# Kernel tuning notes

Hardware: AMD Instinct MI355X
Metric: run time of the kernel (lower is better)

## Reference

```python
import jax, jax.numpy as jnp
import numpy as np

VOCAB = 50000
E = 300        # embedding_dim
HID = 512      # hidden_dim (bidirectional total)
HD = HID // 2  # per-direction hidden
K = 20         # tagset size
START = 18
STOP = 19
B = 64
T = 256
NEG = -10000.0


def setup_inputs() -> dict:
    key = jax.random.key(0)
    ks = jax.random.split(key, 12)
    s = 0.1
    sentence = jax.random.randint(ks[0], (B, T), 0, VOCAB)
    length = jax.random.randint(ks[1], (B,), T // 2, T + 1)
    embed_table = jax.random.normal(ks[2], (VOCAB, E)) * s
    w_ih_f = jax.random.normal(ks[3], (4 * HD, E)) * s
    w_hh_f = jax.random.normal(ks[4], (4 * HD, HD)) * s
    b_f = jax.random.normal(ks[5], (4 * HD,)) * s
    w_ih_b = jax.random.normal(ks[6], (4 * HD, E)) * s
    w_hh_b = jax.random.normal(ks[7], (4 * HD, HD)) * s
    b_b = jax.random.normal(ks[8], (4 * HD,)) * s
    W_out = jax.random.normal(ks[9], (K, HID)) * s
    b_out = jax.random.normal(ks[10], (K,)) * s
    transitions = jax.random.normal(ks[11], (K, K))
    transitions = transitions.at[START, :].set(NEG).at[:, STOP].set(NEG)
    return dict(sentence=sentence, length=length, embed_table=embed_table,
                w_ih_f=w_ih_f, w_hh_f=w_hh_f, b_f=b_f,
                w_ih_b=w_ih_b, w_hh_b=w_hh_b, b_b=b_b,
                W_out=W_out, b_out=b_out, transitions=transitions)


def _lstm(xs, w_ih, w_hh, b, reverse):
    # xs: [T, B, E]; PyTorch gate order i, f, g, o
    Bn = xs.shape[1]
    H = w_hh.shape[1]

    def step(carry, x):
        h, c = carry
        g = x @ w_ih.T + h @ w_hh.T + b
        i, f, gg, o = jnp.split(g, 4, axis=-1)
        c = jax.nn.sigmoid(f) * c + jax.nn.sigmoid(i) * jnp.tanh(gg)
        h = jax.nn.sigmoid(o) * jnp.tanh(c)
        return (h, c), h

    init = (jnp.zeros((Bn, H), xs.dtype), jnp.zeros((Bn, H), xs.dtype))
    _, hs = jax.lax.scan(step, init, xs, reverse=reverse)
    return hs  # [T, B, H], time-ordered


def _viterbi(feats, length, transitions):
    # feats: [B, T, K]; vectorized over batch, scan over time
    Bn, Tn, Kn = feats.shape
    fv0 = jnp.full((Bn, Kn), NEG, feats.dtype).at[:, START].set(0.0)
    idk = jnp.arange(Kn)

    def step(fv, inp):
        feat_t, t = inp
        # scores[b, next, prev] = fv[b, prev] + transitions[next, prev]
        sc = fv[:, None, :] + transitions[None, :, :]
        bp = jnp.argmax(sc, axis=-1)              # [B, K]
        best = jnp.max(sc, axis=-1) + feat_t      # [B, K]
        m = (t < length)[:, None]
        fv_new = jnp.where(m, best, fv)           # freeze past sentence end
        bp = jnp.where(m, bp, idk[None, :])       # identity backpointer on pad
        return fv_new, bp

    fv, bps = jax.lax.scan(step, fv0, (jnp.swapaxes(feats, 0, 1), jnp.arange(Tn)))
    term = fv + transitions[STOP][None, :]
    last = jnp.argmax(term, axis=-1)              # [B]
    score = jnp.max(term, axis=-1)                # [B] viterbi max score

    def back(tag, bp_t):
        prev = jnp.take_along_axis(bp_t, tag[:, None], axis=1)[:, 0]
        return prev, tag

    _, path_t = jax.lax.scan(back, last, bps, reverse=True)  # [T, B], time order
    path = jnp.swapaxes(path_t, 0, 1)             # [B, T]; entries >= length repeat last tag
    return score, path


def reference(sentence, length, embed_table, w_ih_f, w_hh_f, b_f,
              w_ih_b, w_hh_b, b_b, W_out, b_out, transitions):
    embeds = embed_table[sentence]                # [B, T, E]
    xs = jnp.swapaxes(embeds, 0, 1)               # [T, B, E]
    hf = _lstm(xs, w_ih_f, w_hh_f, b_f, reverse=False)
    hb = _lstm(xs, w_ih_b, w_hh_b, b_b, reverse=True)
    h = jnp.concatenate([hf, hb], axis=-1)        # [T, B, HID]
    feats = h @ W_out.T + b_out                   # [T, B, K]
    feats = jnp.swapaxes(feats, 0, 1)             # [B, T, K]
    score, path = _viterbi(feats, length, transitions)
    return score, path
```

## Files before the change

kernel.cpp:

```cpp
#include <hip/hip_runtime.h>
#include <hip/hip_bf16.h>

#define DINL __device__ __forceinline__

namespace {

typedef unsigned long long u64;

constexpr int Tn = 256;
constexpr int Bn = 64;
constexpr int HDn = 256;
constexpr int Kt = 20;
constexpr int STOPt = 19;
constexpr int STARTt = 18;
constexpr float NEGV = -10000.0f;

DINL float sigm(float x) { return 1.0f / (1.0f + __expf(-x)); }
DINL float tanh_f(float x) {
  float ax = fabsf(x);
  float e = __expf(-2.0f * ax);
  float t = (1.0f - e) / (1.0f + e);
  return x < 0.0f ? -t : t;
}

__global__ void k_clear(int4* p) {
  int i = threadIdx.x;
  p[i] = {0, 0, 0, 0};
}

__global__ void k_wt(const float* __restrict__ wf, const float* __restrict__ wb,
                     float* __restrict__ Wt) {
  int idx = blockIdx.x * 256 + threadIdx.x;
  if (idx >= 300 * 2048) return;
  int k = idx >> 11, n = idx & 2047;
  const float* w = (n < 1024) ? wf : wb;
  int nn = n & 1023;
  Wt[idx] = w[nn * 300 + k];
}

__global__ __launch_bounds__(256) void k_xproj(
    const int* __restrict__ sentence, const float* __restrict__ table,
    const float* __restrict__ Wt, const float* __restrict__ b_f,
    const float* __restrict__ b_b, float* __restrict__ xproj) {
  __shared__ float As[20][68];
  __shared__ float Bs[20][136];
  __shared__ int tok[64];

  int tid = threadIdx.x;
  int t = blockIdx.x;
  int n0 = blockIdx.y * 128;

  if (tid < 64) tok[tid] = sentence[tid * Tn + t];
  __syncthreads();

  int ty = tid >> 4, tx = tid & 15;
  float acc[4][8];
#pragma unroll
  for (int i = 0; i < 4; ++i)
#pragma unroll
    for (int j = 0; j < 8; ++j) acc[i][j] = 0.0f;

  for (int k0 = 0; k0 < 300; k0 += 20) {
#pragma unroll
    for (int i = 0; i < 5; ++i) {
      int idx = i * 256 + tid;
      int r = idx / 20, kk = idx % 20;
      As[kk][r] = table[tok[r] * 300 + k0 + kk];
    }
#pragma unroll
    for (int i = 0; i < 10; ++i) {
      int idx = i * 256 + tid;
      int kk = idx >> 7, c = idx & 127;
      Bs[kk][c] = Wt[(k0 + kk) * 2048 + n0 + c];
    }
    __syncthreads();
#pragma unroll
    for (int kk = 0; kk < 20; ++kk) {
      float4 a4 = *(const float4*)&As[kk][ty * 4];
      float4 b4a = *(const float4*)&Bs[kk][tx * 8];
      float4 b4b = *(const float4*)&Bs[kk][tx * 8 + 4];
      float av[4] = {a4.x, a4.y, a4.z, a4.w};
      float bvv[8] = {b4a.x, b4a.y, b4a.z, b4a.w, b4b.x, b4b.y, b4b.z, b4b.w};
#pragma unroll
      for (int i = 0; i < 4; ++i)
#pragma unroll
        for (int j = 0; j < 8; ++j) acc[i][j] += av[i] * bvv[j];
    }
    __syncthreads();
  }

  float bias[8];
#pragma unroll
  for (int j = 0; j < 8; ++j) {
    int n = n0 + tx * 8 + j;
    bias[j] = (n < 1024) ? b_f[n] : b_b[n - 1024];
  }
#pragma unroll
  for (int i = 0; i < 4; ++i) {
    size_t m = (size_t)t * 64 + ty * 4 + i;
    float* dst = &xproj[m * 2048 + n0 + tx * 8];
    float4 v0 = {acc[i][0] + bias[0], acc[i][1] + bias[1], acc[i][2] + bias[2],
                 acc[i][3] + bias[3]};
    float4 v1 = {acc[i][4] + bias[4], acc[i][5] + bias[5], acc[i][6] + bias[6],
                 acc[i][7] + bias[7]};
    *(float4*)dst = v0;
    *(float4*)(dst + 4) = v1;
  }
}

__global__ __launch_bounds__(128) void k_lstm(
    const float* __restrict__ whh_f, const float* __restrict__ whh_b,
    const float* __restrict__ xproj, float* __restrict__ h_all,
    int* __restrict__ flags) {
  __shared__ __align__(16) float hl[16 * 256];

  int tid = threadIdx.x;
  int bid = blockIdx.x;
  int gid = bid & 7;
  int s = bid >> 3;
  int dir = gid >> 2;
  int bg = gid & 3;
  const float* whh = dir ? whh_b : whh_f;

  int c = tid >> 4;
  int kc = tid & 15;

  float4 w4[4][4];
#pragma unroll
  for (int g = 0; g < 4; ++g) {
    const float* src = whh + ((size_t)(g * 256 + s * 8 + c)) * 256;
#pragma unroll
    for (int jj = 0; jj < 4; ++jj)
      w4[g][jj] = *(const float4*)(src + ((kc + (jj << 4)) << 2));
  }

  float c_reg = 0.0f;

  for (int st = 0; st < Tn; ++st) {
    int xt = dir ? (Tn - 1 - st) : st;

    float xp[4];
    {
      size_t base = ((size_t)(xt * 64 + bg * 16 + kc)) * 2048 + dir * 1024 +
                    s * 8 + c;
#pragma unroll
      for (int g = 0; g < 4; ++g) xp[g] = xproj[base + g * 256];
    }

    float acc[16][4];
#pragma unroll
    for (int b = 0; b < 16; ++b)
#pragma unroll
      for (int g = 0; g < 4; ++g) acc[b][g] = 0.0f;

    if (st > 0) {
      if (tid < 64) {
        const int* fp = flags + ((gid << 5) + (tid & 31)) * 4;
        for (;;) {
          int v = __hip_atomic_load(fp, __ATOMIC_RELAXED,
                                    __HIP_MEMORY_SCOPE_AGENT);
          if (__all((tid < 32) ? (v >= st) : 1)) break;
          __builtin_amdgcn_s_sleep(1);
        }
      }
      __syncthreads();

      int pt = dir ? (xt + 1) : (xt - 1);
      const float* hsrc =
          h_all + ((size_t)(dir * Tn + pt) * 64 + bg * 16) * 256;
      const char* tb = (const char*)hsrc + (size_t)tid * 16;
      const char* p0 = tb;
      const char* p1 = tb + 4096;
      const char* p2 = tb + 8192;
      const char* p3 = tb + 12288;
      float4 q0, q1, q2, q3, q4, q5, q6, q7;
      asm volatile(
          "global_load_dwordx4 %0, %8, off sc1\n\t"
          "global_load_dwordx4 %1, %8, off offset:2048 sc1\n\t"
          "global_load_dwordx4 %2, %9, off sc1\n\t"
          "global_load_dwordx4 %3, %9, off offset:2048 sc1\n\t"
          "global_load_dwordx4 %4, %10, off sc1\n\t"
          "global_load_dwordx4 %5, %10, off offset:2048 sc1\n\t"
          "global_load_dwordx4 %6, %11, off sc1\n\t"
          "global_load_dwordx4 %7, %11, off offset:2048 sc1\n\t"
          "s_waitcnt vmcnt(0)"
          : "=&v"(q0), "=&v"(q1), "=&v"(q2), "=&v"(q3), "=&v"(q4), "=&v"(q5),
            "=&v"(q6), "=&v"(q7)
          : "v"(p0), "v"(p1), "v"(p2), "v"(p3));
      *(float4*)&hl[(tid + 0 * 128) << 2] = q0;
      *(float4*)&hl[(tid + 1 * 128) << 2] = q1;
      *(float4*)&hl[(tid + 2 * 128) << 2] = q2;
      *(float4*)&hl[(tid + 3 * 128) << 2] = q3;
      *(float4*)&hl[(tid + 4 * 128) << 2] = q4;
      *(float4*)&hl[(tid + 5 * 128) << 2] = q5;
      *(float4*)&hl[(tid + 6 * 128) << 2] = q6;
      *(float4*)&hl[(tid + 7 * 128) << 2] = q7;
      __syncthreads();

#pragma unroll
      for (int b = 0; b < 16; ++b) {
#pragma unroll
        for (int jj = 0; jj < 4; ++jj) {
          float4 hv = *(const float4*)&hl[b * 256 + ((kc + (jj << 4)) << 2)];
#pragma unroll
          for (int g = 0; g < 4; ++g) {
            acc[b][g] += w4[g][jj].x * hv.x + w4[g][jj].y * hv.y +
                         w4[g][jj].z * hv.z + w4[g][jj].w * hv.w;
          }
        }
      }
    }

#pragma unroll
    for (int r = 0; r < 4; ++r) {
      int m = 1 << r;
      int kb = (kc >> r) & 1;
#pragma unroll
      for (int ii = 0; ii < (16 >> (r + 1)); ++ii) {
#pragma unroll
        for (int g = 0; g < 4; ++g) {
          float e = acc[2 * ii][g], o = acc[2 * ii + 1][g];
          float kept = kb ? o : e;
          float sent = kb ? e : o;
          acc[ii][g] = kept + __shfl_xor(sent, m, 64);
        }
      }
    }

    {
      float gi = acc[0][0] + xp[0];
      float gf = acc[0][1] + xp[1];
      float gg = acc[0][2] + xp[2];
      float go = acc[0][3] + xp[3];
      c_reg = sigm(gf) * c_reg + sigm(gi) * tanh_f(gg);
      float h = sigm(go) * tanh_f(c_reg);
      __hip_atomic_store(
          &h_all[((size_t)(dir * Tn + xt) * 64 + bg * 16 + kc) * 256 + s * 8 +
                 c],
          h, __ATOMIC_RELAXED, __HIP_MEMORY_SCOPE_AGENT);
    }

    asm volatile("s_waitcnt vmcnt(0)" ::: "memory");
    __syncthreads();
    if (tid == 0) {
      __hip_atomic_store(flags + ((gid << 5) + s) * 4, st + 1,
                         __ATOMIC_RELAXED, __HIP_MEMORY_SCOPE_AGENT);
    }
  }
}

__global__ __launch_bounds__(256) void k_feats(const float* __restrict__ h_all,
                                               const float* __restrict__ Wout,
                                               const float* __restrict__ bout,
                                               float* __restrict__ feats) {
  __shared__ float Wl[20 * 512];
  __shared__ float hlf[64 * 256];

  int tid = threadIdx.x;
  int t = blockIdx.x;
  for (int i = tid; i < 20 * 512; i += 256) Wl[i] = Wout[i];

  float acc[5] = {0, 0, 0, 0, 0};
  int b = tid & 63, kg5 = tid >> 6;
  int swz = b & 7;

  for (int d = 0; d < 2; ++d) {
    __syncthreads();
    const float* hsrc = h_all + ((size_t)(d * Tn + t)) * 64 * 256;
#pragma unroll 8
    for (int i = 0; i < 64; ++i) {
      int idx = i * 256 + tid;
      int hb = idx >> 8, k = idx & 255;
      hlf[hb * 256 + 4 * ((k >> 2) ^ (hb & 7)) + (k & 3)] = hsrc[idx];
    }
    __syncthreads();
    for (int jg = 0; jg < 64; ++jg) {
      float4 hv = *(const float4*)&hlf[b * 256 + 4 * (jg ^ swz)];
#pragma unroll
      for (int kk = 0; kk < 5; ++kk) {
        int krow = kg5 * 5 + kk;
        float4 wvv = *(const float4*)&Wl[krow * 512 + d * 256 + jg * 4];
        acc[kk] += hv.x * wvv.x + hv.y * wvv.y + hv.z * wvv.z + hv.w * wvv.w;
      }
    }
  }
#pragma unroll
  for (int kk = 0; kk < 5; ++kk) {
    int krow = kg5 * 5 + kk;
    feats[((size_t)b * Tn + t) * Kt + krow] = acc[kk] + bout[krow];
  }
}

__global__ __launch_bounds__(64) void k_viterbi(const float* __restrict__ feats,
                                                const float* __restrict__ trans,
                                                const int* __restrict__ length,
                                                float* __restrict__ out) {
  __shared__ float tr[400];
  __shared__ float fv[20];
  __shared__ float term[20];
  __shared__ unsigned char bps[256][20];

  int b = blockIdx.x;
  int lane = threadIdx.x;
  for (int i = lane; i < 400; i += 64) tr[i] = trans[i];
  if (lane < 20) fv[lane] = (lane == STARTt) ? 0.0f : NEGV;
  int len = length[b];
  __syncthreads();

  for (int t = 0; t < Tn; ++t) {
    float nf = 0.0f;
    int bp = 0;
    if (lane < 20) {
      if (t < len) {
        float vmax = -3.4e38f;
        int pb = 0;
#pragma unroll
        for (int p = 0; p < 20; ++p) {
          float v = fv[p] + tr[lane * 20 + p];
          if (v > vmax) { vmax = v; pb = p; }
        }
        nf = vmax + feats[((size_t)b * Tn + t) * Kt + lane];
        bp = pb;
      } else {
        nf = fv[lane];
        bp = lane;
      }
    }
    __syncthreads();
    if (lane < 20) {
      fv[lane] = nf;
      bps[t][lane] = (unsigned char)bp;
    }
    __syncthreads();
  }

  if (lane < 20) term[lane] = fv[lane] + tr[STOPt * 20 + lane];
  __syncthreads();
  if (lane == 0) {
    float smax = term[0];
    int last = 0;
    for (int p = 1; p < 20; ++p)
      if (term[p] > smax) { smax = term[p]; last = p; }
    out[b] = smax;
    int tag = last;
    for (int t = Tn - 1; t >= 0; --t) {
      out[64 + b * Tn + t] = (float)tag;
      tag = bps[t][tag];
    }
  }
}

}

extern "C" void kernel_launch(void* const* d_in, const int* in_sizes, int n_in,
                              void* d_out, int out_size, void* d_ws,
                              size_t ws_size, hipStream_t stream) {
  const int* sentence = (const int*)d_in[0];
  const int* length = (const int*)d_in[1];
  const float* table = (const float*)d_in[2];
  const float* w_ih_f = (const float*)d_in[3];
  const float* w_hh_f = (const float*)d_in[4];
  const float* b_f = (const float*)d_in[5];
  const float* w_ih_b = (const float*)d_in[6];
  const float* w_hh_b = (const float*)d_in[7];
  const float* b_b = (const float*)d_in[8];
  const float* W_out = (const float*)d_in[9];
  const float* b_out = (const float*)d_in[10];
  const float* trans = (const float*)d_in[11];
  float* out = (float*)d_out;

  float* ws = (float*)d_ws;
  float* xproj = ws;
  float* h_all = ws + (size_t)33554432;
  float* Wt = h_all + (size_t)8388608;
  float* feats = Wt + (size_t)300 * 2048;
  int* flags = (int*)(feats + (size_t)Bn * Tn * Kt);
  (void)ws_size; (void)in_sizes; (void)n_in; (void)out_size;

  k_clear<<<dim3(1), dim3(512), 0, stream>>>((int4*)flags);
  k_wt<<<dim3(2400), dim3(256), 0, stream>>>(w_ih_f, w_ih_b, Wt);
  k_xproj<<<dim3(256, 16), dim3(256), 0, stream>>>(sentence, table, Wt, b_f,
                                                   b_b, xproj);
  k_lstm<<<dim3(256), dim3(128), 0, stream>>>(w_hh_f, w_hh_b, xproj, h_all,
                                              flags);
  k_feats<<<dim3(256), dim3(256), 0, stream>>>(h_all, W_out, b_out, feats);
  k_viterbi<<<dim3(64), dim3(64), 0, stream>>>(feats, trans, length, out);
}
```

Before: 1.750 ms.

## Use epoch-based flags and plain stores when a sync group shares one XCD

Each LSTM block reads its hardware XCD id and publishes it in a table tagged with a per-launch epoch counter. The 32 blocks of a sync group check whether they all landed on the same XCD, and if so they write h values and progress flags with plain stores instead of agent-scope atomic stores. The flag-clearing kernel is replaced by an epoch increment with epoch-offset flag values, which removes the memset launch. This adds a startup handshake per block and depends on plain stores being visible within one XCD's L2, which is a correctness risk.

```diff
diff --git a/kernel.cpp b/kernel.cpp
--- a/kernel.cpp
+++ b/kernel.cpp
@@ -23,9 +23,9 @@
   return x < 0.0f ? -t : t;
 }
 
-__global__ void k_clear(int4* p) {
-  int i = threadIdx.x;
-  p[i] = {0, 0, 0, 0};
+__global__ void k_epoch(unsigned* ep) {
+  if (threadIdx.x == 0)
+    __hip_atomic_fetch_add(ep, 1u, __ATOMIC_RELAXED, __HIP_MEMORY_SCOPE_AGENT);
 }
 
 __global__ void k_wt(const float* __restrict__ wf, const float* __restrict__ wb,
@@ -111,8 +111,10 @@
 __global__ __launch_bounds__(128) void k_lstm(
     const float* __restrict__ whh_f, const float* __restrict__ whh_b,
     const float* __restrict__ xproj, float* __restrict__ h_all,
-    int* __restrict__ flags) {
+    int* __restrict__ flags, int* __restrict__ xcdtab,
+    const unsigned* __restrict__ ep) {
   __shared__ __align__(16) float hl[16 * 256];
+  __shared__ int fastsh;
 
   int tid = threadIdx.x;
   int bid = blockIdx.x;
@@ -125,6 +127,31 @@
   int c = tid >> 4;
   int kc = tid & 15;
 
+  unsigned E =
+      __hip_atomic_load(ep, __ATOMIC_RELAXED, __HIP_MEMORY_SCOPE_AGENT);
+  unsigned xcd = __builtin_amdgcn_s_getreg((3 << 11) | (0 << 6) | 20) & 0xFu;
+  if (tid == 0) {
+    __hip_atomic_store(&xcdtab[(gid << 5) + s],
+                       (int)((E << 4) | xcd), __ATOMIC_RELAXED,
+                       __HIP_MEMORY_SCOPE_AGENT);
+  }
+  if (tid < 64) {
+    const int* xp_ = xcdtab + (gid << 5) + (tid & 31);
+    unsigned v;
+    for (;;) {
+      v = (unsigned)__hip_atomic_load(xp_, __ATOMIC_RELAXED,
+                                      __HIP_MEMORY_SCOPE_AGENT);
+      bool rdy = (v >> 4) == (E & 0x0FFFFFFFu);
+      if (__all((tid < 32) ? rdy : 1)) break;
+      __builtin_amdgcn_s_sleep(1);
+    }
+    int mine = (int)(v & 0xFu);
+    int ref = __shfl(mine, 0, 64);
+    bool eq = (mine == ref);
+    bool alleq = __all((tid < 32) ? eq : 1);
+    if (tid == 0) fastsh = alleq ? 1 : 0;
+  }
+
   float4 w4[4][4];
 #pragma unroll
   for (int g = 0; g < 4; ++g) {
@@ -134,6 +161,10 @@
       w4[g][jj] = *(const float4*)(src + ((kc + (jj << 4)) << 2));
   }
 
+  __syncthreads();
+  const bool fast = (fastsh != 0);
+  const unsigned base = E * 256u;
+
   float c_reg = 0.0f;
 
   for (int st = 0; st < Tn; ++st) {
@@ -141,10 +172,10 @@
 
     float xp[4];
     {
-      size_t base = ((size_t)(xt * 64 + bg * 16 + kc)) * 2048 + dir * 1024 +
-                    s * 8 + c;
-#pragma unroll
-      for (int g = 0; g < 4; ++g) xp[g] = xproj[base + g * 256];
+      size_t xb = ((size_t)(xt * 64 + bg * 16 + kc)) * 2048 + dir * 1024 +
+                  s * 8 + c;
+#pragma unroll
+      for (int g = 0; g < 4; ++g) xp[g] = xproj[xb + g * 256];
     }
 
     float acc[16][4];
@@ -157,9 +188,10 @@
       if (tid < 64) {
         const int* fp = flags + ((gid << 5) + (tid & 31)) * 4;
         for (;;) {
-          int v = __hip_atomic_load(fp, __ATOMIC_RELAXED,
-                                    __HIP_MEMORY_SCOPE_AGENT);
-          if (__all((tid < 32) ? (v >= st) : 1)) break;
+          unsigned v = (unsigned)__hip_atomic_load(
+              fp, __ATOMIC_RELAXED, __HIP_MEMORY_SCOPE_AGENT);
+          int d = (int)(v - base);
+          if (__all((tid < 32) ? (d >= st) : 1)) break;
           __builtin_amdgcn_s_sleep(1);
         }
       }
@@ -234,17 +266,26 @@
       float go = acc[0][3] + xp[3];
       c_reg = sigm(gf) * c_reg + sigm(gi) * tanh_f(gg);
       float h = sigm(go) * tanh_f(c_reg);
-      __hip_atomic_store(
-          &h_all[((size_t)(dir * Tn + xt) * 64 + bg * 16 + kc) * 256 + s * 8 +
-                 c],
-          h, __ATOMIC_RELAXED, __HIP_MEMORY_SCOPE_AGENT);
+      size_t hi = ((size_t)(dir * Tn + xt) * 64 + bg * 16 + kc) * 256 + s * 8 +
+                  c;
+      if (fast) {
+        h_all[hi] = h;
+      } else {
+        __hip_atomic_store(&h_all[hi], h, __ATOMIC_RELAXED,
+                           __HIP_MEMORY_SCOPE_AGENT);
+      }
     }
 
     asm volatile("s_waitcnt vmcnt(0)" ::: "memory");
     __syncthreads();
     if (tid == 0) {
-      __hip_atomic_store(flags + ((gid << 5) + s) * 4, st + 1,
-                         __ATOMIC_RELAXED, __HIP_MEMORY_SCOPE_AGENT);
+      int fv = (int)(base + (unsigned)(st + 1));
+      if (fast) {
+        flags[((gid << 5) + s) * 4] = fv;
+      } else {
+        __hip_atomic_store(flags + ((gid << 5) + s) * 4, fv, __ATOMIC_RELAXED,
+                           __HIP_MEMORY_SCOPE_AGENT);
+      }
     }
   }
 }
@@ -375,14 +416,16 @@
   float* Wt = h_all + (size_t)8388608;
   float* feats = Wt + (size_t)300 * 2048;
   int* flags = (int*)(feats + (size_t)Bn * Tn * Kt);
+  int* xcdtab = flags + 1024;
+  unsigned* ep = (unsigned*)(xcdtab + 256);
   (void)ws_size; (void)in_sizes; (void)n_in; (void)out_size;
 
-  k_clear<<<dim3(1), dim3(512), 0, stream>>>((int4*)flags);
+  k_epoch<<<dim3(1), dim3(64), 0, stream>>>(ep);
   k_wt<<<dim3(2400), dim3(256), 0, stream>>>(w_ih_f, w_ih_b, Wt);
   k_xproj<<<dim3(256, 16), dim3(256), 0, stream>>>(sentence, table, Wt, b_f,
                                                    b_b, xproj);
   k_lstm<<<dim3(256), dim3(128), 0, stream>>>(w_hh_f, w_hh_b, xproj, h_all,
-                                              flags);
+                                              flags, xcdtab, ep);
   k_feats<<<dim3(256), dim3(256), 0, stream>>>(h_all, W_out, b_out, feats);
   k_viterbi<<<dim3(64), dim3(64), 0, stream>>>(feats, trans, length, out);
 }
```

Result: faster. 1.480 ms (-15.4%).
